# Performance work log

Hardware: AMD Instinct MI355X
Metric: run time of the kernel (lower is better)

Reference implementation:

```python
import jax, jax.numpy as jnp
import numpy as np

D_MODEL = 2048
N_EXPERTS = 8
TOP_K = 2
FFN_HIDDEN = int(D_MODEL * 1.5)  # 3072, matches int(d_model*1.5)


def setup_inputs() -> dict:
    key = jax.random.key(0)
    k_x, k_r, k_g, k_u, k_d = jax.random.split(key, 5)
    B, L = 4, 4096
    s_in = 1.0 / np.sqrt(D_MODEL)
    s_hid = 1.0 / np.sqrt(FFN_HIDDEN)
    return {
        "x": jax.random.normal(k_x, (B, L, D_MODEL), dtype=jnp.float32),
        # nn.Linear weights are stored (out_features, in_features)
        "router_w": jax.random.uniform(k_r, (N_EXPERTS, D_MODEL), jnp.float32, -s_in, s_in),
        "gate_w": jax.random.uniform(k_g, (N_EXPERTS, FFN_HIDDEN, D_MODEL), jnp.float32, -s_in, s_in),
        "up_w": jax.random.uniform(k_u, (N_EXPERTS, FFN_HIDDEN, D_MODEL), jnp.float32, -s_in, s_in),
        "down_w": jax.random.uniform(k_d, (N_EXPERTS, D_MODEL, FFN_HIDDEN), jnp.float32, -s_hid, s_hid),
    }


def reference(x, router_w, gate_w, up_w, down_w):
    B, L, D = x.shape
    x_flat = x.reshape(-1, D)                                   # [N, D]

    router_logits = x_flat @ router_w.T                          # [N, E]
    router_probs = jax.nn.softmax(router_logits, axis=-1)
    top_k_probs, top_k_idx = jax.lax.top_k(router_probs, TOP_K)  # [N, K]
    top_k_probs = top_k_probs / jnp.sum(top_k_probs, axis=-1, keepdims=True)

    # combine[n, e] = sum_k top_k_probs[n,k] * (top_k_idx[n,k] == e)
    onehot = jax.nn.one_hot(top_k_idx, N_EXPERTS, dtype=x.dtype)  # [N, K, E]
    combine = jnp.einsum("nk,nke->ne", top_k_probs, onehot)       # [N, E]

    # Masked gather/scatter in the original == weight-0 tokens here; same math.
    output = jnp.zeros_like(x_flat)
    for e in range(N_EXPERTS):
        gate = jax.nn.silu(x_flat @ gate_w[e].T)                  # [N, H]
        up = x_flat @ up_w[e].T                                   # [N, H]
        expert_out = (gate * up) @ down_w[e].T                    # [N, D]
        output = output + combine[:, e:e + 1] * expert_out

    # dropout is identity in eval/reference mode
    return output.reshape(B, L, D)
```

## Files before the change

kernel.cpp:

```cpp
#include <hip/hip_runtime.h>
#include <hip/hip_bf16.h>
#include <cstdint>

#define N_TOK 16384
#define DMODEL 2048
#define FFH    3072
#define NGU    (2 * FFH)
#define NEXP   8
#define ATOT   32768

typedef __bf16 bf16;
typedef __attribute__((ext_vector_type(8))) __bf16 bf16x8;
typedef __attribute__((ext_vector_type(4))) __bf16 bf16x4;
typedef __attribute__((ext_vector_type(4))) float  f32x4;

__device__ __forceinline__ void gl_lds16(const bf16* g, void* l) {
  __builtin_amdgcn_global_load_lds(
      (const __attribute__((address_space(1))) void*)g,
      (__attribute__((address_space(3))) void*)l, 16, 0, 0);
}

__global__ void cvt_f32_bf16(const float* __restrict__ src, bf16* __restrict__ dst, long n4) {
  long i = (long)blockIdx.x * blockDim.x + threadIdx.x;
  if (i >= n4) return;
  const float4 v = ((const float4*)src)[i];
  bf16x4 o;
  o.x = (bf16)v.x; o.y = (bf16)v.y; o.z = (bf16)v.z; o.w = (bf16)v.w;
  ((bf16x4*)dst)[i] = o;
}

__global__ void cvt_guw(const float* __restrict__ gw, const float* __restrict__ uw,
                        bf16* __restrict__ guw) {
  const long i = (long)blockIdx.x * 256 + threadIdx.x;
  const int c8 = (int)(i & 255);
  const long rg = i >> 8;
  const int e = (int)(rg / NGU);
  const int ri = (int)(rg - (long)e * NGU);
  const int hb = ri >> 6, sub = ri & 63;
  const float* src = (sub < 32 ? gw : uw) + ((size_t)e * FFH + hb * 32 + (sub & 31)) * DMODEL + c8 * 8;
  const float4 v0 = ((const float4*)src)[0];
  const float4 v1 = ((const float4*)src)[1];
  bf16x8 o;
  o[0] = (bf16)v0.x; o[1] = (bf16)v0.y; o[2] = (bf16)v0.z; o[3] = (bf16)v0.w;
  o[4] = (bf16)v1.x; o[5] = (bf16)v1.y; o[6] = (bf16)v1.z; o[7] = (bf16)v1.w;
  *(bf16x8*)(guw + rg * DMODEL + c8 * 8) = o;
}

__global__ void router_k(const float* __restrict__ x, const float* __restrict__ rw,
                         int* __restrict__ tk_e, float* __restrict__ tk_w,
                         int* __restrict__ cnt) {
  const int wv = threadIdx.x >> 6, lane = threadIdx.x & 63;
  const int t = blockIdx.x * 4 + wv;
  const float* xr = x + (size_t)t * DMODEL;
  float acc[NEXP];
#pragma unroll
  for (int e = 0; e < NEXP; ++e) acc[e] = 0.f;
  for (int k = lane; k < DMODEL; k += 64) {
    const float xv = xr[k];
#pragma unroll
    for (int e = 0; e < NEXP; ++e) acc[e] = fmaf(xv, rw[e * DMODEL + k], acc[e]);
  }
#pragma unroll
  for (int e = 0; e < NEXP; ++e) {
#pragma unroll
    for (int o = 32; o; o >>= 1) acc[e] += __shfl_xor(acc[e], o, 64);
  }
  if (lane == 0) {
    int e0 = 0; float v0 = acc[0];
#pragma unroll
    for (int e = 1; e < NEXP; ++e) if (acc[e] > v0) { v0 = acc[e]; e0 = e; }
    int e1 = -1; float v1 = -1e30f;
#pragma unroll
    for (int e = 0; e < NEXP; ++e) if (e != e0 && acc[e] > v1) { v1 = acc[e]; e1 = e; }
    const float w0 = 1.f / (1.f + __expf(v1 - v0));
    tk_e[t * 2] = e0; tk_e[t * 2 + 1] = e1;
    tk_w[t * 2] = w0; tk_w[t * 2 + 1] = 1.f - w0;
    atomicAdd(&cnt[e0], 1); atomicAdd(&cnt[e1], 1);
  }
}

__global__ void offs_k(const int* __restrict__ cnt, int* __restrict__ offs) {
  if (threadIdx.x == 0) {
    int o = 0;
    for (int e = 0; e < NEXP; ++e) { offs[e] = o; o += cnt[e]; }
  }
}

__global__ void scatter_k(const int* __restrict__ tk_e, const float* __restrict__ tk_w,
                          const int* __restrict__ offs, int* __restrict__ cnt2,
                          int* __restrict__ tok_list, float* __restrict__ w_list,
                          int* __restrict__ aidx) {
  const int t = blockIdx.x * 256 + threadIdx.x;
  if (t >= N_TOK) return;
#pragma unroll
  for (int k = 0; k < 2; ++k) {
    const int e = tk_e[t * 2 + k];
    const int p = atomicAdd(&cnt2[e], 1);
    const int a = offs[e] + p;
    tok_list[a] = t;
    w_list[a] = tk_w[t * 2 + k];
    aidx[t * 2 + k] = a;
  }
}

template<int EPI>
__global__ __launch_bounds__(512, 2) void gemm_moe(
    const bf16* __restrict__ A, const bf16* __restrict__ B,
    bf16* __restrict__ hbuf, float* __restrict__ ybuf,
    const int* __restrict__ tok_list, const int* __restrict__ cnt,
    const int* __restrict__ offs) {
  constexpr int KD = EPI ? FFH : DMODEL;
  constexpr int NT = KD / 32;
  constexpr int BROWS = EPI ? DMODEL : NGU;

  const int e = blockIdx.z;
  const int cn = cnt[e];
  const int mbase = blockIdx.y * 256;
  if (mbase >= cn) return;
  const int offE = offs[e];
  const int nbase = blockIdx.x * 256;

  __shared__ char lds[98304];
  char* const ldsA = lds;
  char* const ldsB = lds + 49152;

  const int tid = threadIdx.x;
  const int wv = tid >> 6, lane = tid & 63;
  const int wr = wv >> 2, wc = wv & 3;

  const int sr = tid >> 2;
  const int swz8 = ((tid & 3) ^ ((tid >> 3) & 3)) * 8;
  const bf16* pA[2]; const bf16* pB[2];
  if (EPI == 0) {
    const int t0 = tok_list[offE + min(mbase + sr, cn - 1)];
    const int t1 = tok_list[offE + min(mbase + 128 + sr, cn - 1)];
    pA[0] = A + (size_t)t0 * KD + swz8;
    pA[1] = A + (size_t)t1 * KD + swz8;
  } else {
    const int a0 = offE + min(mbase + sr, cn - 1);
    const int a1 = offE + min(mbase + 128 + sr, cn - 1);
    pA[0] = A + (size_t)a0 * KD + swz8;
    pA[1] = A + (size_t)a1 * KD + swz8;
  }
  pB[0] = B + ((size_t)e * BROWS + nbase + sr) * KD + swz8;
  pB[1] = B + ((size_t)e * BROWS + nbase + 128 + sr) * KD + swz8;

  const int stageDst = wv * 1024;

  const int rswz = ((lane >> 4) ^ ((lane >> 1) & 3)) * 16;
  const int arow = (wr * 128 + (lane & 15)) * 64 + rswz;
  const int brow = (wc * 64 + (lane & 15)) * 64 + rswz;

  const f32x4 zero = {0.f, 0.f, 0.f, 0.f};
  f32x4 acc[8][4];
#pragma unroll
  for (int i = 0; i < 8; ++i)
#pragma unroll
    for (int j = 0; j < 4; ++j) acc[i][j] = zero;

  auto stage_half = [&](int buf, int q, int kt) {
    const int k8 = kt * 32;
    if (q < 2) gl_lds16(pA[q] + k8, ldsA + buf * 16384 + q * 8192 + stageDst);
    else       gl_lds16(pB[q - 2] + k8, ldsB + buf * 16384 + (q - 2) * 8192 + stageDst);
  };

#pragma unroll
  for (int q = 0; q < 4; ++q) stage_half(0, q, 0);
#pragma unroll
  for (int q = 0; q < 4; ++q) stage_half(1, q, 1);
  asm volatile("s_waitcnt vmcnt(4)" ::: "memory");
  __builtin_amdgcn_s_barrier();
  asm volatile("" ::: "memory");

  int cb = 0;
  for (int kt = 0; kt < NT; ++kt) {
    const int sb = (cb + 2 >= 3) ? cb - 1 : cb + 2;
    const char* cA = ldsA + cb * 16384;
    const char* cB = ldsB + cb * 16384;
    bf16x8 bfr[4];
#pragma unroll
    for (int q = 0; q < 4; ++q) {
      const bf16x8 a0 = *(const bf16x8*)(cA + (q * 2) * 1024 + arow);
      const bf16x8 a1 = *(const bf16x8*)(cA + (q * 2 + 1) * 1024 + arow);
      if (q == 0) {
#pragma unroll
        for (int nf = 0; nf < 4; ++nf)
          bfr[nf] = *(const bf16x8*)(cB + nf * 1024 + brow);
      }
      if (kt + 2 < NT) stage_half(sb, q, kt + 2);
      asm volatile("" ::: "memory");
      __builtin_amdgcn_s_barrier();
      asm volatile("" ::: "memory");
      __builtin_amdgcn_s_setprio(1);
#pragma unroll
      for (int nf = 0; nf < 4; ++nf) {
        acc[q * 2][nf]     = __builtin_amdgcn_mfma_f32_16x16x32_bf16(a0, bfr[nf], acc[q * 2][nf], 0, 0, 0);
        acc[q * 2 + 1][nf] = __builtin_amdgcn_mfma_f32_16x16x32_bf16(a1, bfr[nf], acc[q * 2 + 1][nf], 0, 0, 0);
      }
      __builtin_amdgcn_s_setprio(0);
      if (q == 3) {
        if (kt + 2 < NT) { asm volatile("s_waitcnt vmcnt(4)" ::: "memory"); }
        else             { asm volatile("s_waitcnt vmcnt(0)" ::: "memory"); }
      }
      asm volatile("" ::: "memory");
      __builtin_amdgcn_s_barrier();
      asm volatile("" ::: "memory");
    }
    cb = (cb + 1 == 3) ? 0 : cb + 1;
  }

  const int col = lane & 15;
  const int rb = mbase + wr * 128 + (lane >> 4) * 4;
  if (EPI == 0) {
    const int hb32 = ((nbase + wc * 64) >> 6) * 32;
#pragma unroll
    for (int mi = 0; mi < 8; ++mi)
#pragma unroll
      for (int j = 0; j < 4; ++j) {
        const int row = rb + mi * 16 + j;
        if (row < cn) {
          bf16* hr = hbuf + (size_t)(offE + row) * FFH + hb32 + col;
#pragma unroll
          for (int k = 0; k < 2; ++k) {
            const float g = acc[mi][k][j], u = acc[mi][k + 2][j];
            hr[k * 16] = (bf16)(g / (1.f + __expf(-g)) * u);
          }
        }
      }
  } else {
#pragma unroll
    for (int mi = 0; mi < 8; ++mi)
#pragma unroll
      for (int j = 0; j < 4; ++j) {
        const int row = rb + mi * 16 + j;
        if (row < cn) {
          float* yr = ybuf + (size_t)(offE + row) * DMODEL + nbase + wc * 64 + col;
#pragma unroll
          for (int nf = 0; nf < 4; ++nf) yr[nf * 16] = acc[mi][nf][j];
        }
      }
  }
}

__global__ void combine_k(const float* __restrict__ ybuf, const int* __restrict__ aidx,
                          const float* __restrict__ tk_w, float* __restrict__ out) {
  const int i = blockIdx.x * 256 + threadIdx.x;
  const int t = i >> 9, c = i & 511;
  const int a0 = aidx[t * 2], a1 = aidx[t * 2 + 1];
  const float w0 = tk_w[t * 2], w1 = tk_w[t * 2 + 1];
  const float4 v0 = ((const float4*)(ybuf + (size_t)a0 * DMODEL))[c];
  const float4 v1 = ((const float4*)(ybuf + (size_t)a1 * DMODEL))[c];
  float4 o;
  o.x = w0 * v0.x + w1 * v1.x;
  o.y = w0 * v0.y + w1 * v1.y;
  o.z = w0 * v0.z + w1 * v1.z;
  o.w = w0 * v0.w + w1 * v1.w;
  ((float4*)(out + (size_t)t * DMODEL))[c] = o;
}

extern "C" void kernel_launch(void* const* d_in, const int* in_sizes, int n_in,
                              void* d_out, int out_size, void* d_ws, size_t ws_size,
                              hipStream_t stream) {
  const float* x  = (const float*)d_in[0];
  const float* rw = (const float*)d_in[1];
  const float* gw = (const float*)d_in[2];
  const float* uw = (const float*)d_in[3];
  const float* dw = (const float*)d_in[4];
  float* out = (float*)d_out;

  char* ws = (char*)d_ws;
  size_t o = 0;
  auto alloc = [&](size_t bytes) {
    void* p = ws + o;
    o = (o + bytes + 255) & ~(size_t)255;
    return p;
  };

  const size_t guw_bytes  = (size_t)NEXP * NGU * DMODEL * 2;
  const size_t ybuf_bytes = (size_t)(ATOT + 256) * DMODEL * 4;
  bf16*  xb       = (bf16*)alloc((size_t)N_TOK * DMODEL * 2);
  void*  uni      = alloc(ybuf_bytes > guw_bytes ? ybuf_bytes : guw_bytes);
  bf16*  guw      = (bf16*)uni;
  float* ybuf     = (float*)uni;
  bf16*  dwb      = (bf16*)alloc((size_t)NEXP * DMODEL * FFH * 2);
  bf16*  hbuf     = (bf16*)alloc((size_t)(ATOT + 256) * FFH * 2);
  int*   tok_list = (int*)alloc((ATOT + 256) * 4);
  float* w_list   = (float*)alloc((ATOT + 256) * 4);
  int*   tk_e     = (int*)alloc((size_t)N_TOK * 2 * 4);
  float* tk_w     = (float*)alloc((size_t)N_TOK * 2 * 4);
  int*   aidx     = (int*)alloc((size_t)N_TOK * 2 * 4);
  int*   cnt      = (int*)alloc(64);
  int*   offs     = (int*)alloc(64);
  int*   cnt2     = (int*)alloc(64);

  hipMemsetAsync(cnt, 0, 64, stream);
  hipMemsetAsync(cnt2, 0, 64, stream);

  {
    long n4 = (long)N_TOK * DMODEL / 4;
    cvt_f32_bf16<<<(unsigned)(n4 / 256), 256, 0, stream>>>(x, xb, n4);
  }
  cvt_guw<<<(unsigned)((long)NEXP * NGU * DMODEL / 8 / 256), 256, 0, stream>>>(gw, uw, guw);
  {
    long n4 = (long)NEXP * DMODEL * FFH / 4;
    cvt_f32_bf16<<<(unsigned)(n4 / 256), 256, 0, stream>>>(dw, dwb, n4);
  }

  router_k<<<N_TOK / 4, 256, 0, stream>>>(x, rw, tk_e, tk_w, cnt);
  offs_k<<<1, 64, 0, stream>>>(cnt, offs);
  scatter_k<<<N_TOK / 256, 256, 0, stream>>>(tk_e, tk_w, offs, cnt2, tok_list, w_list, aidx);

  gemm_moe<0><<<dim3(NGU / 256, 64, NEXP), 512, 0, stream>>>(
      xb, guw, hbuf, nullptr, tok_list, cnt, offs);
  gemm_moe<1><<<dim3(DMODEL / 256, 64, NEXP), 512, 0, stream>>>(
      hbuf, dwb, nullptr, ybuf, tok_list, cnt, offs);

  combine_k<<<N_TOK * 512 / 256, 256, 0, stream>>>(ybuf, aidx, tk_w, out);
}
```

Measured before the change: 2.059 ms.

## Load whole K-tile fragments up front and cut per-tile barriers to one

The GEMM main loop now reads all A and B fragments for the current LDS buffer at the start of each K-tile, instead of interleaving reads across four sub-steps. The loop then issues MFMAs in two halves with the global-to-LDS staging placed between them, and uses a single barrier per K-tile where there were eight. The aim is to cut barrier synchronisation overhead and give the scheduler larger MFMA blocks. In exchange it needs more registers for fragments, which could lower occupancy, and it depends on the triple-buffer distance to keep LDS reads and writes from racing.

```diff
diff --git a/kernel.cpp b/kernel.cpp
--- a/kernel.cpp
+++ b/kernel.cpp
@@ -177,35 +177,42 @@
     const int sb = (cb + 2 >= 3) ? cb - 1 : cb + 2;
     const char* cA = ldsA + cb * 16384;
     const char* cB = ldsB + cb * 16384;
-    bf16x8 bfr[4];
-#pragma unroll
-    for (int q = 0; q < 4; ++q) {
-      const bf16x8 a0 = *(const bf16x8*)(cA + (q * 2) * 1024 + arow);
-      const bf16x8 a1 = *(const bf16x8*)(cA + (q * 2 + 1) * 1024 + arow);
-      if (q == 0) {
-#pragma unroll
-        for (int nf = 0; nf < 4; ++nf)
-          bfr[nf] = *(const bf16x8*)(cB + nf * 1024 + brow);
-      }
-      if (kt + 2 < NT) stage_half(sb, q, kt + 2);
-      asm volatile("" ::: "memory");
-      __builtin_amdgcn_s_barrier();
-      asm volatile("" ::: "memory");
-      __builtin_amdgcn_s_setprio(1);
-#pragma unroll
-      for (int nf = 0; nf < 4; ++nf) {
-        acc[q * 2][nf]     = __builtin_amdgcn_mfma_f32_16x16x32_bf16(a0, bfr[nf], acc[q * 2][nf], 0, 0, 0);
-        acc[q * 2 + 1][nf] = __builtin_amdgcn_mfma_f32_16x16x32_bf16(a1, bfr[nf], acc[q * 2 + 1][nf], 0, 0, 0);
-      }
-      __builtin_amdgcn_s_setprio(0);
-      if (q == 3) {
-        if (kt + 2 < NT) { asm volatile("s_waitcnt vmcnt(4)" ::: "memory"); }
-        else             { asm volatile("s_waitcnt vmcnt(0)" ::: "memory"); }
-      }
-      asm volatile("" ::: "memory");
-      __builtin_amdgcn_s_barrier();
-      asm volatile("" ::: "memory");
+
+    bf16x8 a[8], b[4];
+#pragma unroll
+    for (int i = 0; i < 4; ++i) {
+      a[i] = *(const bf16x8*)(cA + i * 1024 + arow);
+      b[i] = *(const bf16x8*)(cB + i * 1024 + brow);
     }
+#pragma unroll
+    for (int i = 4; i < 8; ++i) a[i] = *(const bf16x8*)(cA + i * 1024 + arow);
+
+    if (kt + 2 < NT) { stage_half(sb, 0, kt + 2); stage_half(sb, 1, kt + 2); }
+
+    __builtin_amdgcn_s_setprio(1);
+#pragma unroll
+    for (int nf = 0; nf < 4; ++nf)
+#pragma unroll
+      for (int mi = 0; mi < 4; ++mi)
+        acc[mi][nf] = __builtin_amdgcn_mfma_f32_16x16x32_bf16(a[mi], b[nf], acc[mi][nf], 0, 0, 0);
+    __builtin_amdgcn_s_setprio(0);
+
+    if (kt + 2 < NT) { stage_half(sb, 2, kt + 2); stage_half(sb, 3, kt + 2); }
+
+    __builtin_amdgcn_s_setprio(1);
+#pragma unroll
+    for (int nf = 0; nf < 4; ++nf)
+#pragma unroll
+      for (int mi = 4; mi < 8; ++mi)
+        acc[mi][nf] = __builtin_amdgcn_mfma_f32_16x16x32_bf16(a[mi], b[nf], acc[mi][nf], 0, 0, 0);
+    __builtin_amdgcn_s_setprio(0);
+
+    if (kt + 2 < NT) { asm volatile("s_waitcnt vmcnt(4)" ::: "memory"); }
+    else             { asm volatile("s_waitcnt vmcnt(0)" ::: "memory"); }
+    asm volatile("" ::: "memory");
+    __builtin_amdgcn_s_barrier();
+    asm volatile("" ::: "memory");
+
     cb = (cb + 1 == 3) ? 0 : cb + 1;
   }
 
```

After: 1.999 ms. -2.9%, faster.
